# Performance work log

Hardware: AMD Instinct MI355X
Metric: run time of the kernel (lower is better)

The kernel has to match this reference:

```python
import jax, jax.numpy as jnp
import numpy as np

HIDDEN = 128
IN_DIM = 2
OUT_DIM = 3


def _graph_conv(x, src, dst, edge_weight, W_rel, b_rel, W_root, num_nodes):
    # PyG GraphConv: lin_rel(scatter_add(ew * x[src] -> dst)) + lin_root(x)
    msg = x[src] * edge_weight[:, None]                       # [E, C_in]
    aggr = jax.ops.segment_sum(msg, dst, num_segments=num_nodes)  # [N, C_in]
    return aggr @ W_rel + b_rel + x @ W_root                  # [N, C_out]


def setup_inputs() -> dict:
    key = jax.random.key(0)
    ks = jax.random.split(key, 12)
    N, E = 100000, 1600000
    x = jax.random.normal(ks[0], (N, IN_DIM), dtype=jnp.float32)
    edge_index = jax.random.randint(ks[1], (2, E), 0, N, dtype=jnp.int64)
    edge_weight = jax.random.uniform(ks[2], (E,), dtype=jnp.float32)
    batch = jnp.zeros((N,), dtype=jnp.int64)

    def glorot(k, fan_in, fan_out):
        s = jnp.sqrt(1.0 / fan_in).astype(jnp.float32)
        return jax.random.uniform(k, (fan_in, fan_out), jnp.float32, -s, s)

    params = {
        "W1_rel": glorot(ks[3], IN_DIM, HIDDEN),
        "b1_rel": jnp.zeros((HIDDEN,), jnp.float32),
        "W1_root": glorot(ks[4], IN_DIM, HIDDEN),
        "W2_rel": glorot(ks[5], HIDDEN, HIDDEN),
        "b2_rel": jnp.zeros((HIDDEN,), jnp.float32),
        "W2_root": glorot(ks[6], HIDDEN, HIDDEN),
        "W3_rel": glorot(ks[7], HIDDEN, OUT_DIM),
        "b3_rel": jnp.zeros((OUT_DIM,), jnp.float32),
        "W3_root": glorot(ks[8], HIDDEN, OUT_DIM),
    }
    return {"x": x, "edge_index": edge_index, "edge_weight": edge_weight,
            "batch": batch, **params}


def reference(x, edge_index, edge_weight, batch,
              W1_rel, b1_rel, W1_root,
              W2_rel, b2_rel, W2_root,
              W3_rel, b3_rel, W3_root):
    N = x.shape[0]
    src, dst = edge_index[0], edge_index[1]
    h = _graph_conv(x, src, dst, edge_weight, W1_rel, b1_rel, W1_root, N)
    h = jax.nn.relu(h)
    h = _graph_conv(h, src, dst, edge_weight, W2_rel, b2_rel, W2_root, N)
    h = jax.nn.relu(h)
    h = _graph_conv(h, src, dst, edge_weight, W3_rel, b3_rel, W3_root, N)
    return h
```

## Files before the change

### kernel.cpp

```cpp
#include <hip/hip_runtime.h>

#define HIDDEN 128
#define NCHUNK 256
#define CBITS  9

typedef float v2f __attribute__((ext_vector_type(2)));
typedef short short8 __attribute__((ext_vector_type(8)));
typedef float f32x4 __attribute__((ext_vector_type(4)));
__device__ __forceinline__ v2f v2s(float a) { v2f r; r.x = a; r.y = a; return r; }

__device__ __forceinline__ ushort f2bf(float f) {
    uint u = __float_as_uint(f);
    u += 0x7FFFu + ((u >> 16) & 1u);
    return (ushort)(u >> 16);
}
__device__ __forceinline__ float bf2f(ushort h) {
    return __uint_as_float(((uint)h) << 16);
}


__global__ __launch_bounds__(256)
void k_bhist(const int* __restrict__ dst, int* __restrict__ bh, int E, int CS) {
    __shared__ int h[256];
    int c = blockIdx.x;
    h[threadIdx.x] = 0;
    __syncthreads();
    int beg = c * CS, end = min(E, beg + CS);
    for (int e = beg + threadIdx.x; e < end; e += 256)
        atomicAdd(&h[dst[e] >> CBITS], 1);
    __syncthreads();
    bh[c * 256 + threadIdx.x] = h[threadIdx.x];
}

__global__ __launch_bounds__(256)
void k_cscan(const int* __restrict__ bh, int* __restrict__ choff,
             int* __restrict__ bbase) {
    __shared__ int sm[256];
    int b = threadIdx.x;
    int acc = 0;
    for (int c = 0; c < NCHUNK; c += 8) {
        int v[8];
#pragma unroll
        for (int i = 0; i < 8; ++i) v[i] = bh[(c + i) * 256 + b];
#pragma unroll
        for (int i = 0; i < 8; ++i) { choff[(c + i) * 256 + b] = acc; acc += v[i]; }
    }
    int tot = acc;
    sm[b] = tot;
    __syncthreads();
    int run = tot;
    for (int d = 1; d < 256; d <<= 1) {
        int t = (b >= d) ? sm[b - d] : 0;
        __syncthreads();
        run += t;
        sm[b] = run;
        __syncthreads();
    }
    bbase[b] = run - tot;
    if (b == 255) bbase[256] = run;
}

__global__ __launch_bounds__(256)
void k_scatter(const int* __restrict__ src, const int* __restrict__ dst,
               const float* __restrict__ ew, const int* __restrict__ choff,
               const int* __restrict__ bbase, int2* __restrict__ staged,
               int E, int CS) {
    __shared__ int cur[256];
    int c = blockIdx.x;
    cur[threadIdx.x] = bbase[threadIdx.x] + choff[c * 256 + threadIdx.x];
    __syncthreads();
    int beg = c * CS, end = min(E, beg + CS);
    for (int e = beg + threadIdx.x; e < end; e += 256) {
        int d = dst[e];
        int slot = atomicAdd(&cur[d >> CBITS], 1);
        int2 p;
        p.x = src[e] | ((d & 511) << 17);
        p.y = __float_as_int(ew[e]);
        staged[slot] = p;
    }
}

__global__ __launch_bounds__(256)
void k_fine(const int2* __restrict__ staged, const int* __restrict__ bbase,
            int* __restrict__ offs, int2* __restrict__ cpack, int N) {
    __shared__ int fc[512];
    __shared__ int fo[512];
    __shared__ int sm[256];
    int b = blockIdx.x;
    int t = threadIdx.x;
    int ebeg = bbase[b], eend = bbase[b + 1];
    fc[t] = 0; fc[t + 256] = 0;
    __syncthreads();
    for (int e = ebeg + t; e < eend; e += 256)
        atomicAdd(&fc[(staged[e].x >> 17) & 511], 1);
    __syncthreads();
    int a0 = fc[2 * t], a1 = fc[2 * t + 1];
    int s = a0 + a1;
    sm[t] = s;
    __syncthreads();
    int run = s;
    for (int d = 1; d < 256; d <<= 1) {
        int v = (t >= d) ? sm[t - d] : 0;
        __syncthreads();
        run += v;
        sm[t] = run;
        __syncthreads();
    }
    int ex = run - s;
    fo[2 * t] = ex;
    fo[2 * t + 1] = ex + a0;
    __syncthreads();
    int nb0 = b << CBITS;
#pragma unroll
    for (int q = 0; q < 2; ++q) {
        int i = q * 256 + t;
        int node = nb0 + i;
        if (node < N) offs[node] = ebeg + fo[i];
    }
    __syncthreads();
    for (int e = ebeg + t; e < eend; e += 256) {
        int2 p = staged[e];
        int dl = (p.x >> 17) & 511;
        int ls = atomicAdd(&fo[dl], 1);
        int2 q2;
        q2.x = p.x & 0x1FFFF;
        q2.y = p.y;
        cpack[ebeg + ls] = q2;
    }
}

__device__ __forceinline__ int end_of(const int* offs, int i, int N, int E) {
    return (i + 1 < N) ? offs[i + 1] : E;
}

__global__ __launch_bounds__(256)
void k_gather2(const int* __restrict__ offs, const int2* __restrict__ cpack,
               const float* __restrict__ x, float4* __restrict__ yv,
               int N, int E) {
    int i = blockIdx.x * 256 + threadIdx.x;
    if (i >= N) return;
    int start = offs[i], end = end_of(offs, i, N, E);
    float a0 = 0.f, a1 = 0.f;
    for (int j = start; j < end; ++j) {
        int2  p = cpack[j];
        int   s = p.x;
        float w = __int_as_float(p.y);
        float2 xv = *reinterpret_cast<const float2*>(x + (size_t)s * 2);
        a0 = fmaf(w, xv.x, a0);
        a1 = fmaf(w, xv.y, a1);
    }
    float2 xi = *reinterpret_cast<const float2*>(x + (size_t)i * 2);
    yv[i] = make_float4(a0, a1, xi.x, xi.y);
}

#define EDGE4(sK, wK)                                              \
    {                                                              \
        v2f t = B + v2s((sK).x) * WR0 + v2s((sK).y) * WR1          \
                  + v2s((sK).z) * WO0 + v2s((sK).w) * WO1;         \
        t = __builtin_elementwise_max(t, Z);                       \
        acc = acc + v2s(wK) * t;                                   \
    }

__global__ __launch_bounds__(256)
void k_gatherfused(const int* __restrict__ offs, const int2* __restrict__ cpack,
                   const float4* __restrict__ yv,
                   const float* __restrict__ W1rel, const float* __restrict__ b1,
                   const float* __restrict__ W1root,
                   ushort* __restrict__ h_hi, ushort* __restrict__ h_lo,
                   ushort* __restrict__ a_hi, ushort* __restrict__ a_lo,
                   int N, int E) {
    int wv   = (blockIdx.x * 256 + threadIdx.x) >> 6;
    int lane = threadIdx.x & 63;
    if (wv >= N) return;
    wv = __builtin_amdgcn_readfirstlane(wv);

    const int c0 = lane * 2;
    const v2f WR0 = *reinterpret_cast<const v2f*>(W1rel  + c0);
    const v2f WR1 = *reinterpret_cast<const v2f*>(W1rel  + HIDDEN + c0);
    const v2f WO0 = *reinterpret_cast<const v2f*>(W1root + c0);
    const v2f WO1 = *reinterpret_cast<const v2f*>(W1root + HIDDEN + c0);
    const v2f B   = *reinterpret_cast<const v2f*>(b1 + c0);
    const v2f Z   = {0.f, 0.f};

    int start = offs[wv];
    int end   = (wv + 1 < N) ? offs[wv + 1] : E;
    v2f acc = {0.f, 0.f};

    for (int base = start; base < end; base += 64) {
        int nb = min(64, end - base);
        int sx = 0, wb = 0;
        if (lane < nb) {
            int2 p = cpack[base + lane];
            sx = p.x; wb = p.y;
        }
        int k = 0;
        for (; k + 8 <= nb; k += 8) {
            int s0 = __builtin_amdgcn_readlane(sx, k + 0);
            int s1 = __builtin_amdgcn_readlane(sx, k + 1);
            int s2 = __builtin_amdgcn_readlane(sx, k + 2);
            int s3 = __builtin_amdgcn_readlane(sx, k + 3);
            int s4 = __builtin_amdgcn_readlane(sx, k + 4);
            int s5 = __builtin_amdgcn_readlane(sx, k + 5);
            int s6 = __builtin_amdgcn_readlane(sx, k + 6);
            int s7 = __builtin_amdgcn_readlane(sx, k + 7);
            float4 y0 = yv[s0]; float4 y1 = yv[s1];
            float4 y2 = yv[s2]; float4 y3 = yv[s3];
            float4 y4 = yv[s4]; float4 y5 = yv[s5];
            float4 y6 = yv[s6]; float4 y7 = yv[s7];
            float w0 = __int_as_float(__builtin_amdgcn_readlane(wb, k + 0));
            float w1 = __int_as_float(__builtin_amdgcn_readlane(wb, k + 1));
            float w2 = __int_as_float(__builtin_amdgcn_readlane(wb, k + 2));
            float w3 = __int_as_float(__builtin_amdgcn_readlane(wb, k + 3));
            float w4 = __int_as_float(__builtin_amdgcn_readlane(wb, k + 4));
            float w5 = __int_as_float(__builtin_amdgcn_readlane(wb, k + 5));
            float w6 = __int_as_float(__builtin_amdgcn_readlane(wb, k + 6));
            float w7 = __int_as_float(__builtin_amdgcn_readlane(wb, k + 7));
            EDGE4(y0, w0) EDGE4(y1, w1) EDGE4(y2, w2) EDGE4(y3, w3)
            EDGE4(y4, w4) EDGE4(y5, w5) EDGE4(y6, w6) EDGE4(y7, w7)
        }
        for (; k + 4 <= nb; k += 4) {
            int s0 = __builtin_amdgcn_readlane(sx, k + 0);
            int s1 = __builtin_amdgcn_readlane(sx, k + 1);
            int s2 = __builtin_amdgcn_readlane(sx, k + 2);
            int s3 = __builtin_amdgcn_readlane(sx, k + 3);
            float4 y0 = yv[s0]; float4 y1 = yv[s1];
            float4 y2 = yv[s2]; float4 y3 = yv[s3];
            float w0 = __int_as_float(__builtin_amdgcn_readlane(wb, k + 0));
            float w1 = __int_as_float(__builtin_amdgcn_readlane(wb, k + 1));
            float w2 = __int_as_float(__builtin_amdgcn_readlane(wb, k + 2));
            float w3 = __int_as_float(__builtin_amdgcn_readlane(wb, k + 3));
            EDGE4(y0, w0) EDGE4(y1, w1) EDGE4(y2, w2) EDGE4(y3, w3)
        }
        for (; k < nb; ++k) {
            int s0 = __builtin_amdgcn_readlane(sx, k);
            float4 y0 = yv[s0];
            float w0 = __int_as_float(__builtin_amdgcn_readlane(wb, k));
            EDGE4(y0, w0)
        }
    }

    {
        ushort hx = f2bf(acc.x);
        ushort lx = f2bf(acc.x - bf2f(hx));
        ushort hy = f2bf(acc.y);
        ushort ly = f2bf(acc.y - bf2f(hy));
        ushort2 hv2; hv2.x = hx; hv2.y = hy;
        ushort2 lv2; lv2.x = lx; lv2.y = ly;
        *reinterpret_cast<ushort2*>(a_hi + (size_t)wv * HIDDEN + c0) = hv2;
        *reinterpret_cast<ushort2*>(a_lo + (size_t)wv * HIDDEN + c0) = lv2;
    }

    {
        float4 y = yv[wv];
        v2f t = B + v2s(y.x) * WR0 + v2s(y.y) * WR1
                  + v2s(y.z) * WO0 + v2s(y.w) * WO1;
        t = __builtin_elementwise_max(t, Z);
        ushort hx = f2bf(t.x);
        ushort lx = f2bf(t.x - bf2f(hx));
        ushort hy = f2bf(t.y);
        ushort ly = f2bf(t.y - bf2f(hy));
        ushort2 hv2; hv2.x = hx; hv2.y = hy;
        ushort2 lv2; lv2.x = lx; lv2.y = ly;
        *reinterpret_cast<ushort2*>(h_hi + (size_t)wv * HIDDEN + c0) = hv2;
        *reinterpret_cast<ushort2*>(h_lo + (size_t)wv * HIDDEN + c0) = lv2;
    }
}

__global__ __launch_bounds__(256)
void k_splitw(const float* __restrict__ Wrel, const float* __restrict__ Wroot,
              ushort* __restrict__ wThi, ushort* __restrict__ wTlo) {
    int idx = blockIdx.x * 256 + threadIdx.x;
    int k = idx >> 7;
    int n = idx & 127;
    float v = (k < 128) ? Wrel[(size_t)k * HIDDEN + n]
                        : Wroot[(size_t)(k - 128) * HIDDEN + n];
    ushort hb = f2bf(v);
    ushort lb = f2bf(v - bf2f(hb));
    wThi[(size_t)n * 256 + k] = hb;
    wTlo[(size_t)n * 256 + k] = lb;
}

#define BM2 64
#define W3_STRIDE 7
#define XS_LD 40

__global__ __launch_bounds__(256)
void k_node2(const ushort* __restrict__ a_hi, const ushort* __restrict__ a_lo,
             const ushort* __restrict__ h_hi, const ushort* __restrict__ h_lo,
             const ushort* __restrict__ wThi, const ushort* __restrict__ wTlo,
             const float* __restrict__ b,
             const float* __restrict__ W3rel, const float* __restrict__ b3,
             const float* __restrict__ W3root,
             float* __restrict__ z, float* __restrict__ out, int N) {
    __shared__ __align__(16) ushort Xhi[BM2 * XS_LD];
    __shared__ __align__(16) ushort Xlo[BM2 * XS_LD];
    __shared__ __align__(16) ushort Whi[HIDDEN * XS_LD];
    __shared__ __align__(16) ushort Wlo[HIDDEN * XS_LD];
    __shared__ float W3s[HIDDEN * W3_STRIDE];

    const int tid  = threadIdx.x;
    const int lane = tid & 63;
    const int wid  = tid >> 6;
    const int ci   = lane & 15;
    const int kb   = lane >> 4;
    const int nb   = blockIdx.x * BM2;

    if (tid < HIDDEN) {
#pragma unroll
        for (int c = 0; c < 3; ++c) {
            W3s[tid * W3_STRIDE + c]     = W3rel [tid * 3 + c];
            W3s[tid * W3_STRIDE + 3 + c] = W3root[tid * 3 + c];
        }
    }

    f32x4 acc[8];
#pragma unroll
    for (int tile = 0; tile < 8; ++tile) {
        float bb = b[tile * 16 + ci];
        f32x4 v; v[0] = bb; v[1] = bb; v[2] = bb; v[3] = bb;
        acc[tile] = v;
    }

    const int sr  = tid >> 2;
    const int skq = (tid & 3) * 8;

    for (int t = 0; t < 8; ++t) {
        const ushort* Ahi = (t < 4) ? a_hi : h_hi;
        const ushort* Alo = (t < 4) ? a_lo : h_lo;
        const int kc = (t & 3) * 32;

        __syncthreads();
        {
            int gr = nb + sr; if (gr >= N) gr = N - 1;
            size_t gofs = (size_t)gr * HIDDEN + kc + skq;
            *reinterpret_cast<short8*>(&Xhi[sr * XS_LD + skq]) =
                *reinterpret_cast<const short8*>(Ahi + gofs);
            *reinterpret_cast<short8*>(&Xlo[sr * XS_LD + skq]) =
                *reinterpret_cast<const short8*>(Alo + gofs);
        }
#pragma unroll
        for (int q = 0; q < 2; ++q) {
            int idx = q * 256 + tid;
            int n  = idx >> 2;
            int kq = (idx & 3) * 8;
            size_t g = (size_t)n * 256 + t * 32 + kq;
            *reinterpret_cast<short8*>(&Whi[n * XS_LD + kq]) =
                *reinterpret_cast<const short8*>(wThi + g);
            *reinterpret_cast<short8*>(&Wlo[n * XS_LD + kq]) =
                *reinterpret_cast<const short8*>(wTlo + g);
        }
        __syncthreads();

        int rl = wid * 16 + ci;
        short8 afh = *reinterpret_cast<const short8*>(&Xhi[rl * XS_LD + kb * 8]);
        short8 afl = *reinterpret_cast<const short8*>(&Xlo[rl * XS_LD + kb * 8]);
#pragma unroll
        for (int tile = 0; tile < 8; ++tile) {
            int nl = tile * 16 + ci;
            short8 bfh = *reinterpret_cast<const short8*>(&Whi[nl * XS_LD + kb * 8]);
            short8 bfl = *reinterpret_cast<const short8*>(&Wlo[nl * XS_LD + kb * 8]);
            acc[tile] = __builtin_amdgcn_mfma_f32_16x16x32_bf16(afh, bfh, acc[tile], 0, 0, 0);
            acc[tile] = __builtin_amdgcn_mfma_f32_16x16x32_bf16(afh, bfl, acc[tile], 0, 0, 0);
            acc[tile] = __builtin_amdgcn_mfma_f32_16x16x32_bf16(afl, bfh, acc[tile], 0, 0, 0);
        }
    }

    const float b30 = b3[0], b31 = b3[1], b32 = b3[2];
#pragma unroll
    for (int m = 0; m < 4; ++m) {
        int node = nb + wid * 16 + kb * 4 + m;
        float zr0 = 0.f, zr1 = 0.f, zr2 = 0.f;
        float zo0 = 0.f, zo1 = 0.f, zo2 = 0.f;
#pragma unroll
        for (int tile = 0; tile < 8; ++tile) {
            float hv = fmaxf(acc[tile][m], 0.f);
            const float* w3 = &W3s[(tile * 16 + ci) * W3_STRIDE];
            zr0 = fmaf(hv, w3[0], zr0); zr1 = fmaf(hv, w3[1], zr1); zr2 = fmaf(hv, w3[2], zr2);
            zo0 = fmaf(hv, w3[3], zo0); zo1 = fmaf(hv, w3[4], zo1); zo2 = fmaf(hv, w3[5], zo2);
        }
#pragma unroll
        for (int d = 8; d >= 1; d >>= 1) {
            zr0 += __shfl_down(zr0, d, 16);
            zr1 += __shfl_down(zr1, d, 16);
            zr2 += __shfl_down(zr2, d, 16);
            zo0 += __shfl_down(zo0, d, 16);
            zo1 += __shfl_down(zo1, d, 16);
            zo2 += __shfl_down(zo2, d, 16);
        }
        if (ci == 0 && node < N) {
            z[(size_t)node * 3 + 0] = zr0;
            z[(size_t)node * 3 + 1] = zr1;
            z[(size_t)node * 3 + 2] = zr2;
            out[(size_t)node * 3 + 0] = zo0 + b30;
            out[(size_t)node * 3 + 1] = zo1 + b31;
            out[(size_t)node * 3 + 2] = zo2 + b32;
        }
    }
}

__global__ __launch_bounds__(256)
void k_gather3(const int* __restrict__ offs, const int2* __restrict__ cpack,
               const float* __restrict__ z, float* __restrict__ out,
               int N, int E) {
    int i = blockIdx.x * 256 + threadIdx.x;
    if (i >= N) return;
    int start = offs[i], end = end_of(offs, i, N, E);
    float a0 = 0.f, a1 = 0.f, a2 = 0.f;
    for (int j = start; j < end; ++j) {
        int2  p = cpack[j];
        int   s = p.x;
        float w = __int_as_float(p.y);
        const float* zp = z + (size_t)s * 3;
        a0 = fmaf(w, zp[0], a0);
        a1 = fmaf(w, zp[1], a1);
        a2 = fmaf(w, zp[2], a2);
    }
    out[(size_t)i * 3 + 0] += a0;
    out[(size_t)i * 3 + 1] += a1;
    out[(size_t)i * 3 + 2] += a2;
}

extern "C" void kernel_launch(void* const* d_in, const int* in_sizes, int n_in,
                              void* d_out, int out_size, void* d_ws, size_t ws_size,
                              hipStream_t stream) {
    const float* x      = (const float*)d_in[0];
    const int*   ei     = (const int*)  d_in[1];
    const float* ew     = (const float*)d_in[2];
    const float* W1rel  = (const float*)d_in[4];
    const float* b1     = (const float*)d_in[5];
    const float* W1root = (const float*)d_in[6];
    const float* W2rel  = (const float*)d_in[7];
    const float* b2     = (const float*)d_in[8];
    const float* W2root = (const float*)d_in[9];
    const float* W3rel  = (const float*)d_in[10];
    const float* b3     = (const float*)d_in[11];
    const float* W3root = (const float*)d_in[12];
    float* out = (float*)d_out;

    const int N = in_sizes[0] / 2;
    const int E = in_sizes[2];
    const int* src = ei;
    const int* dst = ei + E;

    ushort* h_hi = (ushort*)d_ws;
    ushort* h_lo = h_hi + (size_t)N * HIDDEN;
    ushort* a_hi = h_lo + (size_t)N * HIDDEN;
    ushort* a_lo = a_hi + (size_t)N * HIDDEN;
    int*   offs = (int*)(a_lo + (size_t)N * HIDDEN);
    size_t cpo  = (size_t)(offs + N - (int*)d_ws);
    cpo = (cpo + 1) & ~(size_t)1;
    int2*   cpack = (int2*)((int*)d_ws + cpo);
    size_t yvo  = (size_t)((char*)(cpack + E) - (char*)d_ws);
    yvo = (yvo + 15) & ~(size_t)15;
    float4* yv  = (float4*)((char*)d_ws + yvo);
    float* z  = (float*)yv;
    size_t wto = yvo + ((size_t)N * 3 * sizeof(float) + 15 & ~(size_t)15);
    wto = (wto + 15) & ~(size_t)15;
    ushort* wThi = (ushort*)((char*)d_ws + wto);
    ushort* wTlo = wThi + 128 * 256;

    int2* staged = (int2*)d_ws;
    int*  bh     = (int*)a_hi;
    int*  choff  = bh + 256 * 256;
    int*  bbase  = choff + 256 * 256;

    const int CS = (E + NCHUNK - 1) / NCHUNK;
    const int NB = (N + 511) >> CBITS;

    k_bhist  <<<NCHUNK, 256, 0, stream>>>(dst, bh, E, CS);
    k_cscan  <<<1, 256, 0, stream>>>(bh, choff, bbase);
    k_scatter<<<NCHUNK, 256, 0, stream>>>(src, dst, ew, choff, bbase, staged, E, CS);
    k_fine   <<<NB, 256, 0, stream>>>(staged, bbase, offs, cpack, N);

    k_gather2<<<(N + 255) / 256, 256, 0, stream>>>(offs, cpack, x, yv, N, E);

    {
        long long threads = (long long)N * 64;
        k_gatherfused<<<(int)((threads + 255) / 256), 256, 0, stream>>>(
            offs, cpack, yv, W1rel, b1, W1root, h_hi, h_lo, a_hi, a_lo, N, E);
    }

    k_splitw<<<128, 256, 0, stream>>>(W2rel, W2root, wThi, wTlo);

    k_node2<<<(N + BM2 - 1) / BM2, 256, 0, stream>>>(
        a_hi, a_lo, h_hi, h_lo, wThi, wTlo, b2, W3rel, b3, W3root, z, out, N);

    k_gather3<<<(N + 255) / 256, 256, 0, stream>>>(offs, cpack, z, out, N, E);
}
```

Before: 206.3 us.

## Recompute layer-1 activations inside node GEMM instead of storing them

The gather kernel no longer writes the layer-1 root activations as split bf16 hi/lo arrays. The node GEMM kernel recomputes them on the fly from the packed per-node vector and the layer-1 weights while filling shared-memory tiles. This removes a large write and read of intermediate activations, at the cost of extra ALU work and small weight loads per tile. Workspace layout is reshuffled so z and the transposed weights reuse the freed region.

```diff
diff --git a/kernel.cpp b/kernel.cpp
--- a/kernel.cpp
+++ b/kernel.cpp
@@ -17,7 +17,6 @@
 __device__ __forceinline__ float bf2f(ushort h) {
     return __uint_as_float(((uint)h) << 16);
 }
-
 
 __global__ __launch_bounds__(256)
 void k_bhist(const int* __restrict__ dst, int* __restrict__ bh, int E, int CS) {
@@ -166,7 +165,6 @@
                    const float4* __restrict__ yv,
                    const float* __restrict__ W1rel, const float* __restrict__ b1,
                    const float* __restrict__ W1root,
-                   ushort* __restrict__ h_hi, ushort* __restrict__ h_lo,
                    ushort* __restrict__ a_hi, ushort* __restrict__ a_lo,
                    int N, int E) {
     int wv   = (blockIdx.x * 256 + threadIdx.x) >> 6;
@@ -249,21 +247,6 @@
         *reinterpret_cast<ushort2*>(a_hi + (size_t)wv * HIDDEN + c0) = hv2;
         *reinterpret_cast<ushort2*>(a_lo + (size_t)wv * HIDDEN + c0) = lv2;
     }
-
-    {
-        float4 y = yv[wv];
-        v2f t = B + v2s(y.x) * WR0 + v2s(y.y) * WR1
-                  + v2s(y.z) * WO0 + v2s(y.w) * WO1;
-        t = __builtin_elementwise_max(t, Z);
-        ushort hx = f2bf(t.x);
-        ushort lx = f2bf(t.x - bf2f(hx));
-        ushort hy = f2bf(t.y);
-        ushort ly = f2bf(t.y - bf2f(hy));
-        ushort2 hv2; hv2.x = hx; hv2.y = hy;
-        ushort2 lv2; lv2.x = lx; lv2.y = ly;
-        *reinterpret_cast<ushort2*>(h_hi + (size_t)wv * HIDDEN + c0) = hv2;
-        *reinterpret_cast<ushort2*>(h_lo + (size_t)wv * HIDDEN + c0) = lv2;
-    }
 }
 
 __global__ __launch_bounds__(256)
@@ -286,7 +269,9 @@
 
 __global__ __launch_bounds__(256)
 void k_node2(const ushort* __restrict__ a_hi, const ushort* __restrict__ a_lo,
-             const ushort* __restrict__ h_hi, const ushort* __restrict__ h_lo,
+             const float4* __restrict__ yv,
+             const float* __restrict__ W1rel, const float* __restrict__ b1,
+             const float* __restrict__ W1root,
              const ushort* __restrict__ wThi, const ushort* __restrict__ wTlo,
              const float* __restrict__ b,
              const float* __restrict__ W3rel, const float* __restrict__ b3,
@@ -325,18 +310,47 @@
     const int skq = (tid & 3) * 8;
 
     for (int t = 0; t < 8; ++t) {
-        const ushort* Ahi = (t < 4) ? a_hi : h_hi;
-        const ushort* Alo = (t < 4) ? a_lo : h_lo;
         const int kc = (t & 3) * 32;
 
         __syncthreads();
-        {
+        if (t < 4) {
             int gr = nb + sr; if (gr >= N) gr = N - 1;
             size_t gofs = (size_t)gr * HIDDEN + kc + skq;
             *reinterpret_cast<short8*>(&Xhi[sr * XS_LD + skq]) =
-                *reinterpret_cast<const short8*>(Ahi + gofs);
+                *reinterpret_cast<const short8*>(a_hi + gofs);
             *reinterpret_cast<short8*>(&Xlo[sr * XS_LD + skq]) =
-                *reinterpret_cast<const short8*>(Alo + gofs);
+                *reinterpret_cast<const short8*>(a_lo + gofs);
+        } else {
+            int gr = nb + sr; if (gr >= N) gr = N - 1;
+            float4 y = yv[gr];
+            int c0v = kc + skq;
+            float bb[8], r0a[8], r1a[8], o0a[8], o1a[8];
+            *reinterpret_cast<float4*>(&bb[0])  = *reinterpret_cast<const float4*>(b1 + c0v);
+            *reinterpret_cast<float4*>(&bb[4])  = *reinterpret_cast<const float4*>(b1 + c0v + 4);
+            *reinterpret_cast<float4*>(&r0a[0]) = *reinterpret_cast<const float4*>(W1rel + c0v);
+            *reinterpret_cast<float4*>(&r0a[4]) = *reinterpret_cast<const float4*>(W1rel + c0v + 4);
+            *reinterpret_cast<float4*>(&r1a[0]) = *reinterpret_cast<const float4*>(W1rel + HIDDEN + c0v);
+            *reinterpret_cast<float4*>(&r1a[4]) = *reinterpret_cast<const float4*>(W1rel + HIDDEN + c0v + 4);
+            *reinterpret_cast<float4*>(&o0a[0]) = *reinterpret_cast<const float4*>(W1root + c0v);
+            *reinterpret_cast<float4*>(&o0a[4]) = *reinterpret_cast<const float4*>(W1root + c0v + 4);
+            *reinterpret_cast<float4*>(&o1a[0]) = *reinterpret_cast<const float4*>(W1root + HIDDEN + c0v);
+            *reinterpret_cast<float4*>(&o1a[4]) = *reinterpret_cast<const float4*>(W1root + HIDDEN + c0v + 4);
+            ushort hs[8], ls[8];
+#pragma unroll
+            for (int jj = 0; jj < 8; ++jj) {
+                float v = fmaf(y.x, r0a[jj], bb[jj]);
+                v = fmaf(y.y, r1a[jj], v);
+                v = fmaf(y.z, o0a[jj], v);
+                v = fmaf(y.w, o1a[jj], v);
+                v = fmaxf(v, 0.f);
+                ushort hb2 = f2bf(v);
+                hs[jj] = hb2;
+                ls[jj] = f2bf(v - bf2f(hb2));
+            }
+            *reinterpret_cast<short8*>(&Xhi[sr * XS_LD + skq]) =
+                *reinterpret_cast<short8*>(hs);
+            *reinterpret_cast<short8*>(&Xlo[sr * XS_LD + skq]) =
+                *reinterpret_cast<short8*>(ls);
         }
 #pragma unroll
         for (int q = 0; q < 2; ++q) {
@@ -442,9 +456,8 @@
     const int* src = ei;
     const int* dst = ei + E;
 
-    ushort* h_hi = (ushort*)d_ws;
-    ushort* h_lo = h_hi + (size_t)N * HIDDEN;
-    ushort* a_hi = h_lo + (size_t)N * HIDDEN;
+    ushort* hregion = (ushort*)d_ws;
+    ushort* a_hi = hregion + 2 * (size_t)N * HIDDEN;
     ushort* a_lo = a_hi + (size_t)N * HIDDEN;
     int*   offs = (int*)(a_lo + (size_t)N * HIDDEN);
     size_t cpo  = (size_t)(offs + N - (int*)d_ws);
@@ -453,13 +466,12 @@
     size_t yvo  = (size_t)((char*)(cpack + E) - (char*)d_ws);
     yvo = (yvo + 15) & ~(size_t)15;
     float4* yv  = (float4*)((char*)d_ws + yvo);
-    float* z  = (float*)yv;
-    size_t wto = yvo + ((size_t)N * 3 * sizeof(float) + 15 & ~(size_t)15);
-    wto = (wto + 15) & ~(size_t)15;
+
+    int2* staged = (int2*)d_ws;
+    float* z = (float*)d_ws;
+    size_t wto = ((size_t)N * 3 * sizeof(float) + 63) & ~(size_t)63;
     ushort* wThi = (ushort*)((char*)d_ws + wto);
     ushort* wTlo = wThi + 128 * 256;
-
-    int2* staged = (int2*)d_ws;
     int*  bh     = (int*)a_hi;
     int*  choff  = bh + 256 * 256;
     int*  bbase  = choff + 256 * 256;
@@ -477,13 +489,14 @@
     {
         long long threads = (long long)N * 64;
         k_gatherfused<<<(int)((threads + 255) / 256), 256, 0, stream>>>(
-            offs, cpack, yv, W1rel, b1, W1root, h_hi, h_lo, a_hi, a_lo, N, E);
+            offs, cpack, yv, W1rel, b1, W1root, a_hi, a_lo, N, E);
     }
 
     k_splitw<<<128, 256, 0, stream>>>(W2rel, W2root, wThi, wTlo);
 
     k_node2<<<(N + BM2 - 1) / BM2, 256, 0, stream>>>(
-        a_hi, a_lo, h_hi, h_lo, wThi, wTlo, b2, W3rel, b3, W3root, z, out, N);
+        a_hi, a_lo, yv, W1rel, b1, W1root, wThi, wTlo,
+        b2, W3rel, b3, W3root, z, out, N);
 
     k_gather3<<<(N + 255) / 256, 256, 0, stream>>>(offs, cpack, z, out, N, E);
 }
```

After: 208.8 us. Within noise of the previous version (+1.2%).
